# Optimization experiments

Hardware: AMD Instinct MI355X
Metric: run time of the kernel (lower is better)

The kernel has to match this reference:

```python
import jax, jax.numpy as jnp
from jax import lax
import numpy as np

B, N = 64, 128           # graphs per batch, nodes per graph
MAX_LEVEL = 3
N_TRUNKS, TRUNK_LEN = 32, 32
H, OUT = 256, 10


def setup_inputs() -> dict:
    key = jax.random.key(0)
    ks = jax.random.split(key, 12)
    batch_feature = jax.random.normal(ks[0], (B, N), dtype=jnp.float32)
    trunk_idx = jax.random.randint(ks[1], (MAX_LEVEL, N_TRUNKS, TRUNK_LEN), 0, N, dtype=jnp.int32)
    trunk_len = jax.random.randint(ks[2], (MAX_LEVEL, N_TRUNKS), 1, TRUNK_LEN + 1, dtype=jnp.int32)
    s = 1.0 / np.sqrt(H)
    W_enc = jax.random.uniform(ks[3], (1, H), jnp.float32, -1.0, 1.0)
    b_enc = jax.random.uniform(ks[4], (H,), jnp.float32, -1.0, 1.0)
    W_ih = jax.random.uniform(ks[5], (MAX_LEVEL, 4 * H, H), jnp.float32, -s, s)
    W_hh = jax.random.uniform(ks[6], (MAX_LEVEL, 4 * H, H), jnp.float32, -s, s)
    b_ih = jax.random.uniform(ks[7], (MAX_LEVEL, 4 * H), jnp.float32, -s, s)
    b_hh = jax.random.uniform(ks[8], (MAX_LEVEL, 4 * H), jnp.float32, -s, s)
    W_lin = jax.random.uniform(ks[9], (MAX_LEVEL, H, OUT), jnp.float32, -s, s)
    b_lin = jax.random.uniform(ks[10], (MAX_LEVEL, OUT), jnp.float32, -s, s)
    return {"batch_feature": batch_feature, "trunk_idx": trunk_idx, "trunk_len": trunk_len,
            "W_enc": W_enc, "b_enc": b_enc, "W_ih": W_ih, "W_hh": W_hh,
            "b_ih": b_ih, "b_hh": b_hh, "W_lin": W_lin, "b_lin": b_lin}


def _lstm_scan(seq, W_ih, W_hh, b):
    """seq: [L, M, H] -> all hidden states [L, M, H] (single-layer LSTM, PyTorch gate order i,f,g,o)."""
    M = seq.shape[1]
    Hd = W_hh.shape[1]
    def step(carry, x_t):
        h, c = carry
        gates = x_t @ W_ih.T + h @ W_hh.T + b   # [M, 4H]
        i, f, g, o = jnp.split(gates, 4, axis=-1)
        c = jax.nn.sigmoid(f) * c + jax.nn.sigmoid(i) * jnp.tanh(g)
        h = jax.nn.sigmoid(o) * jnp.tanh(c)
        return (h, c), h
    init = (jnp.zeros((M, Hd), seq.dtype), jnp.zeros((M, Hd), seq.dtype))
    _, hs = lax.scan(step, init, seq)
    return hs


def reference(batch_feature, trunk_idx, trunk_len, W_enc, b_enc, W_ih, W_hh, b_ih, b_hh, W_lin, b_lin):
    Bv, Nv = batch_feature.shape
    Hd = W_enc.shape[1]
    # node encoder on scalar features: x [B*N, 1] @ W_enc [1, H]
    x_attr = (batch_feature.reshape(-1, 1) @ W_enc + b_enc).reshape(Bv, Nv, Hd)
    trunk_len = jnp.maximum(trunk_len, 1)
    score = jnp.zeros((Bv, W_lin.shape[-1]), x_attr.dtype)
    for l in range(trunk_idx.shape[0]):
        idx = trunk_idx[l]                       # [T, L]
        T, L = idx.shape
        seqs = x_attr[:, idx]                    # gather trunks -> [B, T, L, H]
        seqs = seqs.reshape(Bv * T, L, Hd).transpose(1, 0, 2)   # [L, B*T, H]
        hs = _lstm_scan(seqs, W_ih[l], W_hh[l], b_ih[l] + b_hh[l])  # [L, B*T, H]
        lens = jnp.tile(trunk_len[l], Bv)        # [B*T]
        h_last = hs[lens - 1, jnp.arange(Bv * T)]   # hidden at last valid step (== packed h_n)
        h_trunk = h_last.reshape(Bv, T, Hd).sum(axis=1)  # scatter-sum per graph (indices are i repeated T times)
        score = score + h_trunk @ W_lin[l] + b_lin[l]
    return score


if __name__ == "__main__":
    out = reference(**setup_inputs())
    print(out.shape, out.dtype)
```

## Files before the change

kernel.cpp:

```cpp
#include <hip/hip_runtime.h>
#include <hip/hip_bf16.h>
#include <stdint.h>

#define B_   64
#define N_   128
#define H_   256
#define FH   1024
#define NT   32
#define TL   32
#define LV   3
#define OUT_ 10
#define NTRK 96
#define UNITS 384

typedef __attribute__((ext_vector_type(4))) int   int4v;
typedef __attribute__((ext_vector_type(4))) float f32x4;

#define QW  (0.0625f / 127.0f)
#define QH  (1.0f / 127.0f)
#define QS  (QW * QH)
#define L2E 1.442695041f
#define QSI (-L2E * QS)
#define QSG (2.0f * L2E * QS)
#define C2  (2.0f * L2E)

__device__ inline float exp2f_(float x) { return __builtin_amdgcn_exp2f(x); }
__device__ inline float rcpf_(float x)  { return __builtin_amdgcn_rcpf(x); }

__global__ void prep_all(const float* __restrict__ W_enc, const float* __restrict__ b_enc,
                         const float* __restrict__ W_ih, const float* __restrict__ b_ih,
                         const float* __restrict__ b_hh, const float* __restrict__ W_hh,
                         const float* __restrict__ b_lin, const float* __restrict__ W_lin,
                         const int* __restrict__ trunk_len,
                         float* __restrict__ u, float* __restrict__ v,
                         char* __restrict__ whh_i8, float* __restrict__ out,
                         int* __restrict__ sorted, int* __restrict__ counter,
                         float* __restrict__ wlT) {
    int blk = blockIdx.x;
    int tid = threadIdx.x;
    if (blk < 768) {
        int j = blk * 4 + (tid >> 6);
        int lane = tid & 63;
        const float4 w  = ((const float4*)(W_ih + (size_t)j * H_))[lane];
        const float4 we = ((const float4*)W_enc)[lane];
        const float4 be = ((const float4*)b_enc)[lane];
        float du = w.x * we.x + w.y * we.y + w.z * we.z + w.w * we.w;
        float dv = w.x * be.x + w.y * be.y + w.z * be.z + w.w * be.w;
        for (int m = 32; m >= 1; m >>= 1) { du += __shfl_xor(du, m); dv += __shfl_xor(dv, m); }
        if (lane == 0) {
            int g = (j & 1023) >> 8;
            float s = (g == 2) ? (2.0f * L2E) : (-L2E);
            u[j] = s * du;
            v[j] = s * (dv + b_ih[j] + b_hh[j]);
        }
    } else if (blk < 1536) {
        int gid = (blk - 768) * 256 + tid;
        const float4 w = ((const float4*)W_hh)[gid];
        char4 o;
        int a0 = __float2int_rn(w.x * (127.0f / 0.0625f));
        int a1 = __float2int_rn(w.y * (127.0f / 0.0625f));
        int a2 = __float2int_rn(w.z * (127.0f / 0.0625f));
        int a3 = __float2int_rn(w.w * (127.0f / 0.0625f));
        a0 = a0 > 127 ? 127 : (a0 < -127 ? -127 : a0);
        a1 = a1 > 127 ? 127 : (a1 < -127 ? -127 : a1);
        a2 = a2 > 127 ? 127 : (a2 < -127 ? -127 : a2);
        a3 = a3 > 127 ? 127 : (a3 < -127 ? -127 : a3);
        o.x = (char)a0; o.y = (char)a1; o.z = (char)a2; o.w = (char)a3;
        ((char4*)whh_i8)[gid] = o;
        if (gid < B_ * OUT_) {
            int oo = gid % OUT_;
            out[gid] = b_lin[oo] + b_lin[OUT_ + oo] + b_lin[2 * OUT_ + oo];
        }
    } else {
        if (tid < NTRK) {
            int li = trunk_len[tid]; if (li < 1) li = 1;
            int rank = 0;
            for (int j2 = 0; j2 < NTRK; ++j2) {
                int lj = trunk_len[j2]; if (lj < 1) lj = 1;
                rank += (lj > li) || (lj == li && j2 < tid);
            }
            sorted[rank] = tid;
        }
        if (tid == 0) *counter = 0;
        for (int idx = tid; idx < LV * OUT_ * H_; idx += 256) {
            int l = idx / (OUT_ * H_);
            int rem = idx - l * OUT_ * H_;
            int o = rem >> 8;
            int k = rem & 255;
            wlT[idx] = W_lin[((size_t)l * H_ + k) * OUT_ + o];
        }
    }
}

__global__ __launch_bounds__(1024) __attribute__((amdgpu_waves_per_eu(4, 4)))
void lstm_main(const float* __restrict__ bfeat, const int* __restrict__ trunk_idx,
               const int* __restrict__ trunk_len,
               const char* __restrict__ whh_i8,
               const float* __restrict__ u, const float* __restrict__ v,
               const float* __restrict__ wlT, const int* __restrict__ sorted,
               int* __restrict__ counter, float* __restrict__ out) {
    __shared__ __align__(16) char hbuf[2][16][272];
    __shared__ __align__(16) float sbuf[2][16];
    __shared__ int sh_uid;

    const int tid = threadIdx.x;
    const int w = tid >> 6;
    const int lane = tid & 63;
    const int col = lane & 15;
    const int q = lane >> 4;

    int4v z4; z4[0] = 0; z4[1] = 0; z4[2] = 0; z4[3] = 0;
    asm volatile("" : "+v"(z4));

    for (;;) {
        if (tid == 0) sh_uid = atomicAdd(counter, 1);
        __syncthreads();
        const int uid = sh_uid;
        if (uid >= UNITS) break;

        const int r = uid >> 2, qq = uid & 3;
        const int tt = sorted[r];
        const int l = tt >> 5;
        const int b0 = qq * 16;

        int len = trunk_len[tt];
        if (len < 1) len = 1;
        const int* tix = trunk_idx + tt * TL;
        const char* whh_l = whh_i8 + (size_t)l * FH * H_;

        int4v Breg[4][4];
        #pragma unroll
        for (int g = 0; g < 4; ++g) {
            int j = g * 256 + w * 16 + col;
            const char* bp = whh_l + (size_t)j * H_ + q * 16;
            #pragma unroll
            for (int k = 0; k < 4; ++k)
                Breg[g][k] = *(const int4v*)(bp + k * 64);
        }

        float u_r[4], v_r[4];
        {
            const float* u_l = u + l * FH;
            const float* v_l = v + l * FH;
            #pragma unroll
            for (int g = 0; g < 4; ++g) {
                int j = g * 256 + w * 16 + col;
                u_r[g] = u_l[j];
                v_r[g] = v_l[j];
            }
        }

        #pragma unroll
        for (int g = 0; g < 4; ++g) {
            #pragma unroll
            for (int k = 0; k < 4; ++k)
                asm volatile("" : "+v"(Breg[g][k]));
            asm volatile("" : "+v"(u_r[g]), "+v"(v_r[g]));
        }

        float c_r[4];

        if (tid < 16) sbuf[0][tid] = bfeat[(b0 + tid) * N_ + tix[0]];
        __syncthreads();

        {
            if (len > 1 && tid < 16) sbuf[1][tid] = bfeat[(b0 + tid) * N_ + tix[1]];
            f32x4 sv = *(const f32x4*)&sbuf[0][q * 4];
            #pragma unroll
            for (int rg = 0; rg < 4; ++rg) {
                float xi = fmaf(sv[rg], u_r[0], v_r[0]);
                float xg = fmaf(sv[rg], u_r[2], v_r[2]);
                float xo = fmaf(sv[rg], u_r[3], v_r[3]);
                float ei = exp2f_(xi);
                float eg = exp2f_(xg);
                float eo = exp2f_(xo);
                float cn = (eg - 1.0f) * rcpf_((1.0f + ei) * (1.0f + eg));
                c_r[rg] = cn;
                float ec = exp2f_(C2 * cn);
                float hq = 127.0f * (ec - 1.0f) * rcpf_((1.0f + eo) * (1.0f + ec));
                hbuf[1][q * 4 + rg][w * 16 + col] = (char)__float2int_rn(hq);
            }
            __syncthreads();
        }

        for (int p = 1; p < len; ++p) {
            const int ri = p & 1, wi = ri ^ 1;

            if (p + 1 < len && tid < 16)
                sbuf[wi][tid] = bfeat[(b0 + tid) * N_ + tix[p + 1]];

            f32x4 sv = *(const f32x4*)&sbuf[ri][q * 4];

            int4v acc[4];
            #pragma unroll
            for (int k = 0; k < 4; ++k) {
                int4v af = *(const int4v*)&hbuf[ri][col][k * 64 + q * 16];
                if (k == 0) {
                    #pragma unroll
                    for (int g = 0; g < 4; ++g)
                        acc[g] = __builtin_amdgcn_mfma_i32_16x16x64_i8(af, Breg[g][0], z4, 0, 0, 0);
                } else {
                    #pragma unroll
                    for (int g = 0; g < 4; ++g)
                        acc[g] = __builtin_amdgcn_mfma_i32_16x16x64_i8(af, Breg[g][k], acc[g], 0, 0, 0);
                }
            }

            #pragma unroll
            for (int rg = 0; rg < 4; ++rg) {
                float xi = fmaf((float)acc[0][rg], QSI, fmaf(sv[rg], u_r[0], v_r[0]));
                float xf = fmaf((float)acc[1][rg], QSI, fmaf(sv[rg], u_r[1], v_r[1]));
                float xg = fmaf((float)acc[2][rg], QSG, fmaf(sv[rg], u_r[2], v_r[2]));
                float xo = fmaf((float)acc[3][rg], QSI, fmaf(sv[rg], u_r[3], v_r[3]));
                float ei = exp2f_(xi);
                float ef = exp2f_(xf);
                float eg = exp2f_(xg);
                float eo = exp2f_(xo);
                float sf = rcpf_(1.0f + ef);
                float ig = (eg - 1.0f) * rcpf_((1.0f + ei) * (1.0f + eg));
                float cn = fmaf(sf, c_r[rg], ig);
                c_r[rg] = cn;
                float ec = exp2f_(C2 * cn);
                float hq = 127.0f * (ec - 1.0f) * rcpf_((1.0f + eo) * (1.0f + ec));
                hbuf[wi][q * 4 + rg][w * 16 + col] = (char)__float2int_rn(hq);
            }

            __syncthreads();
        }

        const char (*hl)[272] = hbuf[len & 1];
        if (tid < 16 * OUT_) {
            int m = tid / OUT_, o = tid % OUT_;
            const float4* wp = (const float4*)(wlT + ((size_t)l * OUT_ + o) * H_);
            const char4*  hp = (const char4*)hl[m];
            float s = 0.f;
            #pragma unroll 8
            for (int k4 = 0; k4 < 64; ++k4) {
                char4  hc = hp[k4];
                float4 wv = wp[k4];
                s += (float)hc.x * wv.x + (float)hc.y * wv.y
                   + (float)hc.z * wv.z + (float)hc.w * wv.w;
            }
            atomicAdd(&out[(b0 + m) * OUT_ + o], s * QH);
        }
    }
}

extern "C" void kernel_launch(void* const* d_in, const int* in_sizes, int n_in,
                              void* d_out, int out_size, void* d_ws, size_t ws_size,
                              hipStream_t stream) {
    const float* bfeat = (const float*)d_in[0];
    const int*   tidx  = (const int*)d_in[1];
    const int*   tlen  = (const int*)d_in[2];
    const float* W_enc = (const float*)d_in[3];
    const float* b_enc = (const float*)d_in[4];
    const float* W_ih  = (const float*)d_in[5];
    const float* W_hh  = (const float*)d_in[6];
    const float* b_ih  = (const float*)d_in[7];
    const float* b_hh  = (const float*)d_in[8];
    const float* W_lin = (const float*)d_in[9];
    const float* b_lin = (const float*)d_in[10];
    float* out = (float*)d_out;

    char*  whh_i8 = (char*)d_ws;
    float* u = (float*)((char*)d_ws + 786432);
    float* v = (float*)((char*)d_ws + 786432 + 12288);
    int* sorted  = (int*)((char*)d_ws + 811008);
    int* counter = (int*)((char*)d_ws + 811392);
    float* wlT   = (float*)((char*)d_ws + 811520);

    prep_all<<<1537, 256, 0, stream>>>(W_enc, b_enc, W_ih, b_ih, b_hh, W_hh, b_lin,
                                       W_lin, tlen, u, v, whh_i8, out, sorted,
                                       counter, wlT);
    lstm_main<<<256, 1024, 0, stream>>>(bfeat, tidx, tlen, whh_i8, u, v, wlT,
                                        sorted, counter, out);
}
```

Before: 149.2 us.

## Halve LSTM block to 512 threads with two gate column tiles per wave

The LSTM block drops from 16 waves to 8. Each wave now holds two 16-column tiles of the int8 recurrent weights in registers and issues twice as many MFMAs per step. This should cut the cost of the per-step barrier, since fewer waves have to synchronise on each recurrence step. In exchange, register pressure per thread roughly doubles, the serial elementwise work per wave doubles, and fewer waves are available to hide latency.

```diff
diff --git a/kernel.cpp b/kernel.cpp
--- a/kernel.cpp
+++ b/kernel.cpp
@@ -92,7 +92,7 @@
     }
 }
 
-__global__ __launch_bounds__(1024) __attribute__((amdgpu_waves_per_eu(4, 4)))
+__global__ __launch_bounds__(512, 2) __attribute__((amdgpu_waves_per_eu(2, 2)))
 void lstm_main(const float* __restrict__ bfeat, const int* __restrict__ trunk_idx,
                const int* __restrict__ trunk_len,
                const char* __restrict__ whh_i8,
@@ -108,6 +108,7 @@
     const int lane = tid & 63;
     const int col = lane & 15;
     const int q = lane >> 4;
+    const int srow = w + ((lane >> 5) << 3);
 
     int4v z4; z4[0] = 0; z4[1] = 0; z4[2] = 0; z4[3] = 0;
     asm volatile("" : "+v"(z4));
@@ -128,102 +129,115 @@
         const int* tix = trunk_idx + tt * TL;
         const char* whh_l = whh_i8 + (size_t)l * FH * H_;
 
-        int4v Breg[4][4];
+        int4v Breg[4][2][4];
         #pragma unroll
-        for (int g = 0; g < 4; ++g) {
-            int j = g * 256 + w * 16 + col;
-            const char* bp = whh_l + (size_t)j * H_ + q * 16;
-            #pragma unroll
-            for (int k = 0; k < 4; ++k)
-                Breg[g][k] = *(const int4v*)(bp + k * 64);
-        }
-
-        float u_r[4], v_r[4];
+        for (int g = 0; g < 4; ++g)
+            #pragma unroll
+            for (int t = 0; t < 2; ++t) {
+                int j = g * 256 + (2 * w + t) * 16 + col;
+                const char* bp = whh_l + (size_t)j * H_ + q * 16;
+                #pragma unroll
+                for (int k = 0; k < 4; ++k)
+                    Breg[g][t][k] = *(const int4v*)(bp + k * 64);
+            }
+
+        float u_r[4][2], v_r[4][2];
         {
             const float* u_l = u + l * FH;
             const float* v_l = v + l * FH;
             #pragma unroll
-            for (int g = 0; g < 4; ++g) {
-                int j = g * 256 + w * 16 + col;
-                u_r[g] = u_l[j];
-                v_r[g] = v_l[j];
-            }
+            for (int g = 0; g < 4; ++g)
+                #pragma unroll
+                for (int t = 0; t < 2; ++t) {
+                    int j = g * 256 + (2 * w + t) * 16 + col;
+                    u_r[g][t] = u_l[j];
+                    v_r[g][t] = v_l[j];
+                }
         }
 
         #pragma unroll
-        for (int g = 0; g < 4; ++g) {
-            #pragma unroll
-            for (int k = 0; k < 4; ++k)
-                asm volatile("" : "+v"(Breg[g][k]));
-            asm volatile("" : "+v"(u_r[g]), "+v"(v_r[g]));
-        }
-
-        float c_r[4];
-
-        if (tid < 16) sbuf[0][tid] = bfeat[(b0 + tid) * N_ + tix[0]];
+        for (int g = 0; g < 4; ++g)
+            #pragma unroll
+            for (int t = 0; t < 2; ++t)
+                #pragma unroll
+                for (int k = 0; k < 4; ++k)
+                    asm volatile("" : "+v"(Breg[g][t][k]));
+
+        float c_r[4][2];
+
+        if ((lane & 31) == 0) sbuf[0][srow] = bfeat[(b0 + srow) * N_ + tix[0]];
         __syncthreads();
 
         {
-            if (len > 1 && tid < 16) sbuf[1][tid] = bfeat[(b0 + tid) * N_ + tix[1]];
+            if (len > 1 && (lane & 31) == 0)
+                sbuf[1][srow] = bfeat[(b0 + srow) * N_ + tix[1]];
             f32x4 sv = *(const f32x4*)&sbuf[0][q * 4];
             #pragma unroll
-            for (int rg = 0; rg < 4; ++rg) {
-                float xi = fmaf(sv[rg], u_r[0], v_r[0]);
-                float xg = fmaf(sv[rg], u_r[2], v_r[2]);
-                float xo = fmaf(sv[rg], u_r[3], v_r[3]);
-                float ei = exp2f_(xi);
-                float eg = exp2f_(xg);
-                float eo = exp2f_(xo);
-                float cn = (eg - 1.0f) * rcpf_((1.0f + ei) * (1.0f + eg));
-                c_r[rg] = cn;
-                float ec = exp2f_(C2 * cn);
-                float hq = 127.0f * (ec - 1.0f) * rcpf_((1.0f + eo) * (1.0f + ec));
-                hbuf[1][q * 4 + rg][w * 16 + col] = (char)__float2int_rn(hq);
-            }
+            for (int t = 0; t < 2; ++t)
+                #pragma unroll
+                for (int rg = 0; rg < 4; ++rg) {
+                    float xi = fmaf(sv[rg], u_r[0][t], v_r[0][t]);
+                    float xg = fmaf(sv[rg], u_r[2][t], v_r[2][t]);
+                    float xo = fmaf(sv[rg], u_r[3][t], v_r[3][t]);
+                    float ei = exp2f_(xi);
+                    float eg = exp2f_(xg);
+                    float eo = exp2f_(xo);
+                    float cn = (eg - 1.0f) * rcpf_((1.0f + ei) * (1.0f + eg));
+                    c_r[rg][t] = cn;
+                    float ec = exp2f_(C2 * cn);
+                    float hq = 127.0f * (ec - 1.0f) * rcpf_((1.0f + eo) * (1.0f + ec));
+                    hbuf[1][q * 4 + rg][(2 * w + t) * 16 + col] = (char)__float2int_rn(hq);
+                }
             __syncthreads();
         }
 
         for (int p = 1; p < len; ++p) {
             const int ri = p & 1, wi = ri ^ 1;
 
-            if (p + 1 < len && tid < 16)
-                sbuf[wi][tid] = bfeat[(b0 + tid) * N_ + tix[p + 1]];
+            if (p + 1 < len && (lane & 31) == 0)
+                sbuf[wi][srow] = bfeat[(b0 + srow) * N_ + tix[p + 1]];
 
             f32x4 sv = *(const f32x4*)&sbuf[ri][q * 4];
 
-            int4v acc[4];
+            int4v acc[4][2];
             #pragma unroll
             for (int k = 0; k < 4; ++k) {
                 int4v af = *(const int4v*)&hbuf[ri][col][k * 64 + q * 16];
                 if (k == 0) {
                     #pragma unroll
                     for (int g = 0; g < 4; ++g)
-                        acc[g] = __builtin_amdgcn_mfma_i32_16x16x64_i8(af, Breg[g][0], z4, 0, 0, 0);
+                        #pragma unroll
+                        for (int t = 0; t < 2; ++t)
+                            acc[g][t] = __builtin_amdgcn_mfma_i32_16x16x64_i8(af, Breg[g][t][0], z4, 0, 0, 0);
                 } else {
                     #pragma unroll
                     for (int g = 0; g < 4; ++g)
-                        acc[g] = __builtin_amdgcn_mfma_i32_16x16x64_i8(af, Breg[g][k], acc[g], 0, 0, 0);
-                }
-            }
-
-            #pragma unroll
-            for (int rg = 0; rg < 4; ++rg) {
-                float xi = fmaf((float)acc[0][rg], QSI, fmaf(sv[rg], u_r[0], v_r[0]));
-                float xf = fmaf((float)acc[1][rg], QSI, fmaf(sv[rg], u_r[1], v_r[1]));
-                float xg = fmaf((float)acc[2][rg], QSG, fmaf(sv[rg], u_r[2], v_r[2]));
-                float xo = fmaf((float)acc[3][rg], QSI, fmaf(sv[rg], u_r[3], v_r[3]));
-                float ei = exp2f_(xi);
-                float ef = exp2f_(xf);
-                float eg = exp2f_(xg);
-                float eo = exp2f_(xo);
-                float sf = rcpf_(1.0f + ef);
-                float ig = (eg - 1.0f) * rcpf_((1.0f + ei) * (1.0f + eg));
-                float cn = fmaf(sf, c_r[rg], ig);
-                c_r[rg] = cn;
-                float ec = exp2f_(C2 * cn);
-                float hq = 127.0f * (ec - 1.0f) * rcpf_((1.0f + eo) * (1.0f + ec));
-                hbuf[wi][q * 4 + rg][w * 16 + col] = (char)__float2int_rn(hq);
-            }
+                        #pragma unroll
+                        for (int t = 0; t < 2; ++t)
+                            acc[g][t] = __builtin_amdgcn_mfma_i32_16x16x64_i8(af, Breg[g][t][k], acc[g][t], 0, 0, 0);
+                }
+            }
+
+            #pragma unroll
+            for (int t = 0; t < 2; ++t)
+                #pragma unroll
+                for (int rg = 0; rg < 4; ++rg) {
+                    float xi = fmaf((float)acc[0][t][rg], QSI, fmaf(sv[rg], u_r[0][t], v_r[0][t]));
+                    float xf = fmaf((float)acc[1][t][rg], QSI, fmaf(sv[rg], u_r[1][t], v_r[1][t]));
+                    float xg = fmaf((float)acc[2][t][rg], QSG, fmaf(sv[rg], u_r[2][t], v_r[2][t]));
+                    float xo = fmaf((float)acc[3][t][rg], QSI, fmaf(sv[rg], u_r[3][t], v_r[3][t]));
+                    float ei = exp2f_(xi);
+                    float ef = exp2f_(xf);
+                    float eg = exp2f_(xg);
+                    float eo = exp2f_(xo);
+                    float sf = rcpf_(1.0f + ef);
+                    float ig = (eg - 1.0f) * rcpf_((1.0f + ei) * (1.0f + eg));
+                    float cn = fmaf(sf, c_r[rg][t], ig);
+                    c_r[rg][t] = cn;
+                    float ec = exp2f_(C2 * cn);
+                    float hq = 127.0f * (ec - 1.0f) * rcpf_((1.0f + eo) * (1.0f + ec));
+                    hbuf[wi][q * 4 + rg][(2 * w + t) * 16 + col] = (char)__float2int_rn(hq);
+                }
 
             __syncthreads();
         }
@@ -272,6 +286,6 @@
     prep_all<<<1537, 256, 0, stream>>>(W_enc, b_enc, W_ih, b_ih, b_hh, W_hh, b_lin,
                                        W_lin, tlen, u, v, whh_i8, out, sorted,
                                        counter, wlT);
-    lstm_main<<<256, 1024, 0, stream>>>(bfeat, tidx, tlen, whh_i8, u, v, wlT,
-                                        sorted, counter, out);
+    lstm_main<<<256, 512, 0, stream>>>(bfeat, tidx, tlen, whh_i8, u, v, wlT,
+                                       sorted, counter, out);
 }
```

After: 153.0 us. 1.03x slower.
